# Kernel tuning notes

Hardware: AMD Instinct MI355X
Metric: run time of the kernel (lower is better)

Reference implementation:

```python
import jax, jax.numpy as jnp
import numpy as np

B = 4096
HASH_BITS = 128
TEACHER_DIM = 768
TEMPERATURE = 0.2
CONTRASTIVE_W = 1.0
DISTILL_W = 0.5
QUANT_W = 0.01


def _l2_normalize(x, eps=1e-12):
    # matches torch F.normalize(dim=-1)
    n = jnp.sqrt(jnp.sum(x * x, axis=-1, keepdims=True))
    return x / jnp.maximum(n, eps)


def setup_inputs() -> dict:
    key = jax.random.key(0)
    k1, k2, k3, k4 = jax.random.split(key, 4)
    logits = jax.random.normal(k1, (B, HASH_BITS), dtype=jnp.float32)
    # binary {-1,+1} codes as in the module contract
    hash_codes = jnp.sign(jax.random.normal(k2, (B, HASH_BITS), dtype=jnp.float32))
    hash_codes = jnp.where(hash_codes == 0, 1.0, hash_codes)
    teacher_embed = jax.random.normal(k3, (B, TEACHER_DIM), dtype=jnp.float32)
    # sparse random positives plus self-positives (guarantees each row nonempty)
    rand_pos = jax.random.uniform(k4, (B, B)) < 0.002
    eye = jnp.eye(B, dtype=bool)
    positive_mask = rand_pos | eye
    return {
        "logits": logits,
        "hash_codes": hash_codes,
        "teacher_embed": teacher_embed,
        "positive_mask": positive_mask,
    }


def reference(logits, hash_codes, teacher_embed, positive_mask):
    teacher = _l2_normalize(teacher_embed)

    # ---- contrastive (vectorized form of the per-row python loop) ----
    ln = _l2_normalize(logits)
    sim = (ln @ ln.T) / TEMPERATURE  # [B, B]
    eye = jnp.eye(sim.shape[0], dtype=bool)
    sim_masked = jnp.where(eye, -jnp.inf, sim)
    # per-row stable logsumexp over self-masked similarities
    log_denom = jax.nn.logsumexp(sim_masked, axis=1)  # [B]
    pm = positive_mask.astype(sim.dtype)
    cnt = pm.sum(axis=1)  # [B]
    pos_mean = (sim * pm).sum(axis=1) / jnp.maximum(cnt, 1.0)
    has_pos = cnt > 0
    per_row = jnp.where(has_pos, -pos_mean + log_denom, 0.0)
    num_pos = jnp.maximum(has_pos.sum(), 1)
    loss_cont = per_row.sum() / num_pos.astype(sim.dtype)

    # ---- distillation: hash similarity vs teacher similarity MSE ----
    hash_sim = (hash_codes @ hash_codes.T) / hash_codes.shape[-1]
    teacher_sim = teacher @ teacher.T
    loss_distill = jnp.mean((hash_sim - teacher_sim) ** 2)

    # ---- quantization: push |logits| toward 1 ----
    loss_quant = jnp.mean(jnp.abs(jnp.abs(logits) - 1.0))

    total = (
        CONTRASTIVE_W * loss_cont
        + DISTILL_W * loss_distill
        + QUANT_W * loss_quant
    )
    return total
```

## Files before the change

### kernel.cpp

```cpp
#include <hip/hip_runtime.h>


typedef __bf16 bf16x8 __attribute__((ext_vector_type(8)));
typedef float f32x4 __attribute__((ext_vector_type(4)));

__device__ __forceinline__ unsigned short f2bf(float f) {
  union { float f; unsigned int u; } v; v.f = f;
  unsigned int u = v.u;
  return (unsigned short)((u + 0x7FFFu + ((u >> 16) & 1u)) >> 16);
}

__device__ __forceinline__ void atomAddF(float* p, float v) {
  unsafeAtomicAdd(p, v);
}

__global__ __launch_bounds__(256) void prep(const float* __restrict__ logits,
                                            const float* __restrict__ hash,
                                            const float* __restrict__ teacher,
                                            unsigned short* __restrict__ P,
                                            unsigned char* __restrict__ QT,
                                            float* __restrict__ qpart,
                                            float* __restrict__ rowexp,
                                            float* __restrict__ possum,
                                            float* __restrict__ cntw,
                                            float* __restrict__ accs,
                                            float* __restrict__ Cbuf) {
  __shared__ float rnt[8];
  __shared__ unsigned char QL[8 * 897];
  const int t = threadIdx.x, wave = t >> 6, lane = t & 63;
  const int r0 = (int)blockIdx.x * 8;

  for (int i = t; i < 224; i += 256)
    *(f32x4*)&Cbuf[((size_t)blockIdx.x * 224 + i) * 4] = (f32x4){0.f, 0.f, 0.f, 0.f};
  if (blockIdx.x == 0) {
    if (t < 4) accs[t] = 0.f;
    if (t == 4) *(int*)&accs[4] = 0;
  }

#pragma unroll
  for (int rr = 0; rr < 2; ++rr) {
    const int rl = wave * 2 + rr, r = r0 + rl;
    float ss = 0.f;
#pragma unroll
    for (int i = 0; i < 3; ++i) {
      const float4 v = *(const float4*)&teacher[(size_t)r * 768 + i * 256 + lane * 4];
      ss += v.x * v.x + v.y * v.y + v.z * v.z + v.w * v.w;
    }
    const float2 lv = *(const float2*)&logits[(size_t)r * 128 + lane * 2];
    float ssl = lv.x * lv.x + lv.y * lv.y;
    float qv = fabsf(fabsf(lv.x) - 1.f) + fabsf(fabsf(lv.y) - 1.f);
#pragma unroll
    for (int off = 1; off < 64; off <<= 1) {
      ss += __shfl_xor(ss, off, 64);
      ssl += __shfl_xor(ssl, off, 64);
      qv += __shfl_xor(qv, off, 64);
    }
    const float rnl = 1.f / fmaxf(sqrtf(ssl), 1e-12f);
    const unsigned int pk = (unsigned int)f2bf(lv.x * rnl) |
                            ((unsigned int)f2bf(lv.y * rnl) << 16);
    *(unsigned int*)&P[(size_t)r * 128 + lane * 2] = pk;
    if (lane == 0) {
      rnt[rl] = 11.313708498984761f / fmaxf(sqrtf(ss), 1e-12f);
      qpart[r] = qv;
    }
  }
  if (t < 8) { rowexp[r0 + t] = 0.f; possum[r0 + t] = 0.f; cntw[r0 + t] = 0.f; }
  __syncthreads();

#pragma unroll
  for (int it = 0; it < 2; ++it) {
    const int task = it * 256 + t;
    if (task < 448) {
      const int r = task / 56, cb = task % 56;
      const int r_g = r0 + r;
      unsigned char* dst = &QL[r * 897 + cb * 16];
      if (cb < 8) {
        const float4 v0 = *(const float4*)&hash[(size_t)r_g * 128 + cb * 16];
        const float4 v1 = *(const float4*)&hash[(size_t)r_g * 128 + cb * 16 + 4];
        const float4 v2 = *(const float4*)&hash[(size_t)r_g * 128 + cb * 16 + 8];
        const float4 v3 = *(const float4*)&hash[(size_t)r_g * 128 + cb * 16 + 12];
        const float vv[16] = {v0.x, v0.y, v0.z, v0.w, v1.x, v1.y, v1.z, v1.w,
                              v2.x, v2.y, v2.z, v2.w, v3.x, v3.y, v3.z, v3.w};
#pragma unroll
        for (int k = 0; k < 16; ++k) dst[k] = vv[k] >= 0.f ? 0x38 : 0xB8;
      } else {
        const float sc = rnt[r];
        const int c0 = cb * 16 - 128;
        const float4 v0 = *(const float4*)&teacher[(size_t)r_g * 768 + c0];
        const float4 v1 = *(const float4*)&teacher[(size_t)r_g * 768 + c0 + 4];
        const float4 v2 = *(const float4*)&teacher[(size_t)r_g * 768 + c0 + 8];
        const float4 v3 = *(const float4*)&teacher[(size_t)r_g * 768 + c0 + 12];
        const float vv[16] = {v0.x, v0.y, v0.z, v0.w, v1.x, v1.y, v1.z, v1.w,
                              v2.x, v2.y, v2.z, v2.w, v3.x, v3.y, v3.z, v3.w};
#pragma unroll
        for (int k = 0; k < 16; ++k) {
          const int p8 = __builtin_amdgcn_cvt_pk_fp8_f32(vv[k] * sc, vv[k] * sc,
                                                         0, false);
          dst[k] = (unsigned char)(p8 & 0xFF);
        }
      }
    }
  }
  __syncthreads();

#pragma unroll
  for (int i = 0; i < 4; ++i) {
    const int c = t + 256 * i;
    if (c < 896) {
      unsigned char buf[8];
#pragma unroll
      for (int j = 0; j < 8; ++j) buf[j] = QL[j * 897 + c];
      *(uint2*)&QT[(size_t)c * 4096 + r0] = *(uint2*)buf;
    }
  }
}

#define STAGE_GEN(GA, GB, PITCH, BASE)                                         \
  {                                                                            \
    _Pragma("unroll") for (int it = 0; it < 4; ++it) {                         \
      const int task = it * 256 + t;                                           \
      const int row = task >> 3;                                               \
      const int c16 = (task & 7) ^ (row & 7);                                  \
      const unsigned char* gpA = (GA) + (size_t)row * (PITCH) + c16 * 16;      \
      __builtin_amdgcn_global_load_lds(                                        \
          (const __attribute__((address_space(1))) void*)gpA,                  \
          (__attribute__((address_space(3))) void*)                            \
              &SB[(BASE) + it * 4096 + wave * 1024],                           \
          16, 0, 0);                                                           \
      if (offdiag) {                                                           \
        const unsigned char* gpB = (GB) + (size_t)row * (PITCH) + c16 * 16;    \
        __builtin_amdgcn_global_load_lds(                                      \
            (const __attribute__((address_space(1))) void*)gpB,                \
            (__attribute__((address_space(3))) void*)                         \
                &SB[(BASE) + 16384 + it * 4096 + wave * 1024],                 \
            16, 0, 0);                                                         \
      }                                                                        \
    }                                                                          \
  }

#define MFMA_B(BASE)                                                           \
  {                                                                            \
    _Pragma("unroll") for (int ks = 0; ks < 2; ++ks) {                         \
      const int ph = ((ks * 4 + qd) ^ (l15 & 7)) * 16;                         \
      bf16x8 af[4], bfr[4];                                                    \
      _Pragma("unroll") for (int rt = 0; rt < 4; ++rt)                         \
          af[rt] = *(const bf16x8*)&SB[(BASE) +                                \
                                       (wy * 64 + rt * 16 + l15) * 128 + ph];  \
      _Pragma("unroll") for (int ct = 0; ct < 4; ++ct)                         \
          bfr[ct] = *(const bf16x8*)&SB[(BASE) + boffB +                       \
                                        (wx * 64 + ct * 16 + l15) * 128 + ph]; \
      _Pragma("unroll") for (int rt = 0; rt < 4; ++rt)                         \
          _Pragma("unroll") for (int ct = 0; ct < 4; ++ct) acc[rt][ct] =       \
          __builtin_amdgcn_mfma_f32_16x16x32_bf16(af[rt], bfr[ct],             \
                                                  acc[rt][ct], 0, 0, 0);       \
    }                                                                          \
  }

#define MFMA_Q(BASE)                                                           \
  {                                                                            \
    _Pragma("unroll") for (int ks = 0; ks < 4; ++ks) {                         \
      const int g0 = ks * 4 + qd;                                              \
      const int ph = ((g0 >> 1) ^ (l15 & 7)) * 16 + (g0 & 1) * 8;              \
      long af[4], bfr[4];                                                      \
      _Pragma("unroll") for (int rt = 0; rt < 4; ++rt)                         \
          af[rt] = *(const long*)&SB[(BASE) +                                  \
                                     (wy * 64 + rt * 16 + l15) * 128 + ph];    \
      _Pragma("unroll") for (int ct = 0; ct < 4; ++ct)                         \
          bfr[ct] = *(const long*)&SB[(BASE) + boffB +                         \
                                      (wx * 64 + ct * 16 + l15) * 128 + ph];   \
      _Pragma("unroll") for (int rt = 0; rt < 4; ++rt)                         \
          _Pragma("unroll") for (int ct = 0; ct < 4; ++ct) acc[rt][ct] =       \
          __builtin_amdgcn_mfma_f32_16x16x32_fp8_fp8(af[rt], bfr[ct],          \
                                                     acc[rt][ct], 0, 0, 0);    \
    }                                                                          \
  }

__global__ __launch_bounds__(256, 2) void mega(const unsigned short* __restrict__ P,
                                               const unsigned char* __restrict__ QT,
                                               const void* __restrict__ mask,
                                               float* __restrict__ rowexp,
                                               float* __restrict__ possum,
                                               float* __restrict__ cntw,
                                               float* __restrict__ Cbuf) {
  __shared__ __align__(16) unsigned char SB[65536];
  __shared__ float redrow[128][2];

  const int t = threadIdx.x;
  const int wave = t >> 6, lane = t & 63;
  const int qd = lane >> 4, l15 = lane & 15;
  const int wy = wave >> 1, wx = wave & 1;
  const int b = (int)blockIdx.x;

  f32x4 acc[4][4];
#pragma unroll
  for (int rt = 0; rt < 4; ++rt)
#pragma unroll
    for (int ct = 0; ct < 4; ++ct) acc[rt][ct] = {0.f, 0.f, 0.f, 0.f};

  if (b < 112) {
    const int tile = b >> 2, ksl = b & 3;
    int I = 0, rem = tile;
    while (rem >= 7 - I) { rem -= 7 - I; ++I; }
    const int J = I + rem;
    const bool offdiag = (I != J);
    const int boffB = offdiag ? 16384 : 0;
    const unsigned char* QA = QT + (size_t)I * 128 * 4096 + ksl * 1024;
    const unsigned char* QB = QT + (size_t)J * 128 * 4096 + ksl * 1024;

    STAGE_GEN(QA, QB, 4096, 0);
    __syncthreads();
    for (int kc = 0; kc < 8; ++kc) {
      const int cb = (kc & 1) * 32768;
      if (kc < 7) STAGE_GEN(QA + (kc + 1) * 128, QB + (kc + 1) * 128, 4096,
                            cb ^ 32768);
      MFMA_Q(cb);
      __syncthreads();
    }
    float* Ct = Cbuf + (size_t)tile * 16384;
#pragma unroll
    for (int rt = 0; rt < 4; ++rt)
#pragma unroll
      for (int ct = 0; ct < 4; ++ct)
#pragma unroll
        for (int i = 0; i < 4; ++i)
          atomAddF(&Ct[(rt * 4 + ct) * 1024 + i * 256 + t], acc[rt][ct][i]);
  } else {
    const int bb = b - 112;
    const int l = (bb & 7) * 128 + (bb >> 3);
    const int bi = l >> 5, bj = l & 31;
    const int ti = bi * 128, tj = bj * 128;
    const bool offdiag = (bi != bj);
    const int boffB = offdiag ? 16384 : 0;
    const bool is_byte = ((const unsigned char*)mask)[4097] != 0;

    const unsigned char* Pa = (const unsigned char*)(P + (size_t)ti * 128);
    const unsigned char* Pb = (const unsigned char*)(P + (size_t)tj * 128);

    STAGE_GEN(Pa, Pb, 256, 0);
    __syncthreads();
    STAGE_GEN(Pa + 128, Pb + 128, 256, 32768);
    MFMA_B(0);
    __syncthreads();
    if (is_byte) {
      const unsigned char* m8d = (const unsigned char*)mask + (size_t)ti * 4096 + tj;
#pragma unroll
      for (int it = 0; it < 4; ++it) {
        const int task = it * 256 + t;
        const int row = task >> 3, seg = task & 7;
        __builtin_amdgcn_global_load_lds(
            (const __attribute__((address_space(1))) void*)
                (m8d + (size_t)row * 4096 + seg * 16),
            (__attribute__((address_space(3))) void*)&SB[it * 4096 + wave * 1024],
            16, 0, 0);
      }
    }
    MFMA_B(32768);
    __syncthreads();
    if (!is_byte) {
      const unsigned int* m32 = (const unsigned int*)mask;
#pragma unroll
      for (int it = 0; it < 16; ++it) {
        const int task = it * 256 + t;
        const int row = task >> 5, seg = task & 31;
        const uint4 v = *(const uint4*)&m32[(size_t)(ti + row) * 4096 + tj + seg * 4];
        uchar4 pk;
        pk.x = v.x ? 1 : 0; pk.y = v.y ? 1 : 0;
        pk.z = v.z ? 1 : 0; pk.w = v.w ? 1 : 0;
        *(uchar4*)&SB[row * 128 + seg * 4] = pk;
      }
      __syncthreads();
    }

#pragma unroll
    for (int rt = 0; rt < 4; ++rt) {
#pragma unroll
      for (int r = 0; r < 4; ++r) {
        const int mrow = wy * 64 + rt * 16 + qd * 4 + r;
        const int m = ti + mrow;
        float se = 0.f;
#pragma unroll
        for (int ct = 0; ct < 4; ++ct) {
          const int ncol = wx * 64 + ct * 16 + l15;
          const int n = tj + ncol;
          const float sim = acc[rt][ct][r] * 5.0f;
          const float e = __expf(sim);
          if (m != n) se += e;
          if (SB[mrow * 128 + ncol]) {
            atomAddF(&possum[m], sim);
            atomAddF(&cntw[m], 1.0f);
          }
        }
#pragma unroll
        for (int off = 1; off < 16; off <<= 1) se += __shfl_xor(se, off, 64);
        if (l15 == 0) redrow[mrow][wx] = se;
      }
    }
    __syncthreads();
    if (t < 128) atomAddF(&rowexp[ti + t], redrow[t][0] + redrow[t][1]);
  }
}

__global__ __launch_bounds__(256) void reduce(const float* __restrict__ rowexp,
                                              const float* __restrict__ possum,
                                              const float* __restrict__ cnt,
                                              const float* __restrict__ qpart,
                                              const float* __restrict__ Cbuf,
                                              float* __restrict__ accs,
                                              float* __restrict__ out) {
  const int t = threadIdx.x;
  const int wave = t >> 6, lane = t & 63;
  const int g = (int)blockIdx.x * 256 + t;

  float c = 0.f, q = 0.f, d = 0.f;
  if (g < 4096) {
    c = logf(rowexp[g]) - possum[g] / fmaxf(cnt[g], 1.0f);
    q = qpart[g];
  }
#pragma unroll
  for (int k = 0; k < 7; ++k) {
    const int e4 = g + k * 16384;
    const int tile = e4 >> 12;
    int I = 0, rem = tile;
    while (rem >= 7 - I) { rem -= 7 - I; ++I; }
    const int J = I + rem;
    const float w = (I == J ? 1.f : 2.f) * (((I == 0) == (J == 0)) ? 1.f : -1.f);
    const f32x4 v = *(const f32x4*)&Cbuf[(size_t)e4 * 4];
    d += w * (v[0] * v[0] + v[1] * v[1] + v[2] * v[2] + v[3] * v[3]);
  }
#pragma unroll
  for (int off = 1; off < 64; off <<= 1) {
    c += __shfl_xor(c, off, 64);
    q += __shfl_xor(q, off, 64);
    d += __shfl_xor(d, off, 64);
  }
  __shared__ float sc[4], sq[4], sd[4];
  if (lane == 0) { sc[wave] = c; sq[wave] = q; sd[wave] = d; }
  __syncthreads();
  if (t == 0) {
    atomAddF(&accs[0], sc[0] + sc[1] + sc[2] + sc[3]);
    atomAddF(&accs[1], sq[0] + sq[1] + sq[2] + sq[3]);
    atomAddF(&accs[2], sd[0] + sd[1] + sd[2] + sd[3]);
    __threadfence();
    const int old = atomicAdd((int*)&accs[4], 1);
    if (old == 63) {
      __threadfence();
      const float C = unsafeAtomicAdd(&accs[0], 0.f);
      const float Q = unsafeAtomicAdd(&accs[1], 0.f);
      const float D = unsafeAtomicAdd(&accs[2], 0.f);
      out[0] = C * (1.0f / 4096.0f) + 0.5f * (D * 3.6379788e-12f) +
               0.01f * (Q * (1.0f / 524288.0f));
    }
  }
}

extern "C" void kernel_launch(void* const* d_in, const int* in_sizes, int n_in,
                              void* d_out, int out_size, void* d_ws, size_t ws_size,
                              hipStream_t stream) {
  const float* logits = (const float*)d_in[0];
  const float* hash = (const float*)d_in[1];
  const float* teacher = (const float*)d_in[2];
  const void* mask = d_in[3];
  float* out = (float*)d_out;

  char* ws = (char*)d_ws;
  float* rowexp = (float*)(ws + 0);
  float* possum = (float*)(ws + 16384);
  float* cntw = (float*)(ws + 32768);
  float* qpart = (float*)(ws + 49152);
  float* accs = (float*)(ws + 65536);
  unsigned short* P = (unsigned short*)(ws + 98304);
  unsigned char* QT = (unsigned char*)(ws + 98304 + 1048576);
  float* Cbuf = (float*)(ws + 98304 + 1048576 + 3670016);

  prep<<<512, 256, 0, stream>>>(logits, hash, teacher, P, QT, qpart, rowexp,
                                possum, cntw, accs, Cbuf);
  mega<<<1136, 256, 0, stream>>>(P, QT, mask, rowexp, possum, cntw, Cbuf);
  reduce<<<64, 256, 0, stream>>>(rowexp, possum, cntw, qpart, Cbuf, accs, out);
}
```

Measured before the change: 151.9 us.

## Fuse final reduction into mega kernel via last-block atomic counters

```diff
diff --git a/kernel.cpp b/kernel.cpp
--- a/kernel.cpp
+++ b/kernel.cpp
@@ -12,6 +12,9 @@
 
 __device__ __forceinline__ void atomAddF(float* p, float v) {
   unsafeAtomicAdd(p, v);
+}
+__device__ __forceinline__ float atomReadF(float* p) {
+  return unsafeAtomicAdd(p, 0.f);
 }
 
 __global__ __launch_bounds__(256) void prep(const float* __restrict__ logits,
@@ -24,6 +27,8 @@
                                             float* __restrict__ possum,
                                             float* __restrict__ cntw,
                                             float* __restrict__ accs,
+                                            int* __restrict__ gcnt,
+                                            int* __restrict__ tileCnt,
                                             float* __restrict__ Cbuf) {
   __shared__ float rnt[8];
   __shared__ unsigned char QL[8 * 897];
@@ -33,8 +38,9 @@
   for (int i = t; i < 224; i += 256)
     *(f32x4*)&Cbuf[((size_t)blockIdx.x * 224 + i) * 4] = (f32x4){0.f, 0.f, 0.f, 0.f};
   if (blockIdx.x == 0) {
-    if (t < 4) accs[t] = 0.f;
-    if (t == 4) *(int*)&accs[4] = 0;
+    if (t < 28) tileCnt[t] = 0;
+    if (t == 28) *gcnt = 0;
+    if (t == 29) accs[0] = 0.f;
   }
 
 #pragma unroll
@@ -181,9 +187,16 @@
                                                float* __restrict__ rowexp,
                                                float* __restrict__ possum,
                                                float* __restrict__ cntw,
-                                               float* __restrict__ Cbuf) {
+                                               const float* __restrict__ qpart,
+                                               float* __restrict__ accs,
+                                               int* __restrict__ gcnt,
+                                               int* __restrict__ tileCnt,
+                                               float* __restrict__ Cbuf,
+                                               float* __restrict__ out) {
   __shared__ __align__(16) unsigned char SB[65536];
   __shared__ float redrow[128][2];
+  __shared__ float red4s[4];
+  __shared__ int flagS;
 
   const int t = threadIdx.x;
   const int wave = t >> 6, lane = t & 63;
@@ -224,6 +237,27 @@
 #pragma unroll
         for (int i = 0; i < 4; ++i)
           atomAddF(&Ct[(rt * 4 + ct) * 1024 + i * 256 + t], acc[rt][ct][i]);
+
+    __threadfence();
+    if (t == 0) flagS = atomicAdd(&tileCnt[tile], 1);
+    __syncthreads();
+    if (flagS == 3) {
+      __threadfence();
+      const float w = (I == J ? 1.f : 2.f) *
+                      (((I == 0) == (J == 0)) ? 1.f : -1.f);
+      float d = 0.f;
+      for (int i = t; i < 16384; i += 256) {
+        const float v = atomReadF(&Ct[i]);
+        d += v * v;
+      }
+      d *= w;
+#pragma unroll
+      for (int off = 1; off < 64; off <<= 1) d += __shfl_xor(d, off, 64);
+      if (lane == 0) red4s[wave] = d;
+      __syncthreads();
+      if (t == 0) atomAddF(&accs[0], red4s[0] + red4s[1] + red4s[2] + red4s[3]);
+    }
+    __syncthreads();
   } else {
     const int bb = b - 112;
     const int l = (bb & 7) * 128 + (bb >> 3);
@@ -298,55 +332,31 @@
     __syncthreads();
     if (t < 128) atomAddF(&rowexp[ti + t], redrow[t][0] + redrow[t][1]);
   }
-}
-
-__global__ __launch_bounds__(256) void reduce(const float* __restrict__ rowexp,
-                                              const float* __restrict__ possum,
-                                              const float* __restrict__ cnt,
-                                              const float* __restrict__ qpart,
-                                              const float* __restrict__ Cbuf,
-                                              float* __restrict__ accs,
-                                              float* __restrict__ out) {
-  const int t = threadIdx.x;
-  const int wave = t >> 6, lane = t & 63;
-  const int g = (int)blockIdx.x * 256 + t;
-
-  float c = 0.f, q = 0.f, d = 0.f;
-  if (g < 4096) {
-    c = logf(rowexp[g]) - possum[g] / fmaxf(cnt[g], 1.0f);
-    q = qpart[g];
-  }
-#pragma unroll
-  for (int k = 0; k < 7; ++k) {
-    const int e4 = g + k * 16384;
-    const int tile = e4 >> 12;
-    int I = 0, rem = tile;
-    while (rem >= 7 - I) { rem -= 7 - I; ++I; }
-    const int J = I + rem;
-    const float w = (I == J ? 1.f : 2.f) * (((I == 0) == (J == 0)) ? 1.f : -1.f);
-    const f32x4 v = *(const f32x4*)&Cbuf[(size_t)e4 * 4];
-    d += w * (v[0] * v[0] + v[1] * v[1] + v[2] * v[2] + v[3] * v[3]);
-  }
-#pragma unroll
-  for (int off = 1; off < 64; off <<= 1) {
-    c += __shfl_xor(c, off, 64);
-    q += __shfl_xor(q, off, 64);
-    d += __shfl_xor(d, off, 64);
-  }
-  __shared__ float sc[4], sq[4], sd[4];
-  if (lane == 0) { sc[wave] = c; sq[wave] = q; sd[wave] = d; }
+
+  __threadfence();
+  if (t == 0) flagS = atomicAdd(gcnt, 1);
   __syncthreads();
-  if (t == 0) {
-    atomAddF(&accs[0], sc[0] + sc[1] + sc[2] + sc[3]);
-    atomAddF(&accs[1], sq[0] + sq[1] + sq[2] + sq[3]);
-    atomAddF(&accs[2], sd[0] + sd[1] + sd[2] + sd[3]);
+  if (flagS == 1135) {
     __threadfence();
-    const int old = atomicAdd((int*)&accs[4], 1);
-    if (old == 63) {
-      __threadfence();
-      const float C = unsafeAtomicAdd(&accs[0], 0.f);
-      const float Q = unsafeAtomicAdd(&accs[1], 0.f);
-      const float D = unsafeAtomicAdd(&accs[2], 0.f);
+    float c = 0.f, q = 0.f;
+    for (int m = t; m < 4096; m += 256) {
+      const float re = atomReadF(&rowexp[m]);
+      const float ps = atomReadF(&possum[m]);
+      const float cn = atomReadF(&cntw[m]);
+      c += logf(re) - ps / fmaxf(cn, 1.0f);
+      q += qpart[m];
+    }
+#pragma unroll
+    for (int off = 1; off < 64; off <<= 1) {
+      c += __shfl_xor(c, off, 64);
+      q += __shfl_xor(q, off, 64);
+    }
+    if (lane == 0) { red4s[wave] = c; redrow[wave][0] = q; }
+    __syncthreads();
+    if (t == 0) {
+      const float C = red4s[0] + red4s[1] + red4s[2] + red4s[3];
+      const float Q = redrow[0][0] + redrow[1][0] + redrow[2][0] + redrow[3][0];
+      const float D = atomReadF(&accs[0]);
       out[0] = C * (1.0f / 4096.0f) + 0.5f * (D * 3.6379788e-12f) +
                0.01f * (Q * (1.0f / 524288.0f));
     }
@@ -368,12 +378,14 @@
   float* cntw = (float*)(ws + 32768);
   float* qpart = (float*)(ws + 49152);
   float* accs = (float*)(ws + 65536);
+  int* gcnt = (int*)(ws + 65600);
+  int* tileCnt = (int*)(ws + 65664);
   unsigned short* P = (unsigned short*)(ws + 98304);
   unsigned char* QT = (unsigned char*)(ws + 98304 + 1048576);
   float* Cbuf = (float*)(ws + 98304 + 1048576 + 3670016);
 
   prep<<<512, 256, 0, stream>>>(logits, hash, teacher, P, QT, qpart, rowexp,
-                                possum, cntw, accs, Cbuf);
-  mega<<<1136, 256, 0, stream>>>(P, QT, mask, rowexp, possum, cntw, Cbuf);
-  reduce<<<64, 256, 0, stream>>>(rowexp, possum, cntw, qpart, Cbuf, accs, out);
-}
+                                possum, cntw, accs, gcnt, tileCnt, Cbuf);
+  mega<<<1136, 256, 0, stream>>>(P, QT, mask, rowexp, possum, cntw, qpart,
+                                 accs, gcnt, tileCnt, Cbuf, out);
+}
```

Result: slower. 233.2 us (+53.6%).

## Exploit symmetry of contrastive similarity to compute only upper-triangle tiles

Applied to the files above, without the earlier changes.

```diff
diff --git a/kernel.cpp b/kernel.cpp
--- a/kernel.cpp
+++ b/kernel.cpp
@@ -12,6 +12,9 @@
 
 __device__ __forceinline__ void atomAddF(float* p, float v) {
   unsafeAtomicAdd(p, v);
+}
+__device__ __forceinline__ float atomReadF(float* p) {
+  return unsafeAtomicAdd(p, 0.f);
 }
 
 __global__ __launch_bounds__(256) void prep(const float* __restrict__ logits,
@@ -184,6 +187,7 @@
                                                float* __restrict__ Cbuf) {
   __shared__ __align__(16) unsigned char SB[65536];
   __shared__ float redrow[128][2];
+  __shared__ float redcol[128][2];
 
   const int t = threadIdx.x;
   const int wave = t >> 6, lane = t & 63;
@@ -226,8 +230,10 @@
           atomAddF(&Ct[(rt * 4 + ct) * 1024 + i * 256 + t], acc[rt][ct][i]);
   } else {
     const int bb = b - 112;
-    const int l = (bb & 7) * 128 + (bb >> 3);
-    const int bi = l >> 5, bj = l & 31;
+    const int l = (bb & 7) * 66 + (bb >> 3);
+    int I = 0, rem = l;
+    while (rem >= 32 - I) { rem -= 32 - I; ++I; }
+    const int bi = I, bj = I + rem;
     const int ti = bi * 128, tj = bj * 128;
     const bool offdiag = (bi != bj);
     const int boffB = offdiag ? 16384 : 0;
@@ -242,7 +248,9 @@
     MFMA_B(0);
     __syncthreads();
     if (is_byte) {
-      const unsigned char* m8d = (const unsigned char*)mask + (size_t)ti * 4096 + tj;
+      const unsigned char* m8 = (const unsigned char*)mask;
+      const unsigned char* m8d = m8 + (size_t)ti * 4096 + tj;
+      const unsigned char* m8t = m8 + (size_t)tj * 4096 + ti;
 #pragma unroll
       for (int it = 0; it < 4; ++it) {
         const int task = it * 256 + t;
@@ -252,6 +260,13 @@
                 (m8d + (size_t)row * 4096 + seg * 16),
             (__attribute__((address_space(3))) void*)&SB[it * 4096 + wave * 1024],
             16, 0, 0);
+        if (offdiag)
+          __builtin_amdgcn_global_load_lds(
+              (const __attribute__((address_space(1))) void*)
+                  (m8t + (size_t)row * 4096 + seg * 16),
+              (__attribute__((address_space(3))) void*)
+                  &SB[16384 + it * 4096 + wave * 1024],
+              16, 0, 0);
       }
     }
     MFMA_B(32768);
@@ -267,10 +282,18 @@
         pk.x = v.x ? 1 : 0; pk.y = v.y ? 1 : 0;
         pk.z = v.z ? 1 : 0; pk.w = v.w ? 1 : 0;
         *(uchar4*)&SB[row * 128 + seg * 4] = pk;
+        if (offdiag) {
+          const uint4 w = *(const uint4*)&m32[(size_t)(tj + row) * 4096 + ti + seg * 4];
+          uchar4 pw;
+          pw.x = w.x ? 1 : 0; pw.y = w.y ? 1 : 0;
+          pw.z = w.z ? 1 : 0; pw.w = w.w ? 1 : 0;
+          *(uchar4*)&SB[16384 + row * 128 + seg * 4] = pw;
+        }
       }
       __syncthreads();
     }
 
+    float ce[4] = {0.f, 0.f, 0.f, 0.f};
 #pragma unroll
     for (int rt = 0; rt < 4; ++rt) {
 #pragma unroll
@@ -285,18 +308,35 @@
           const float sim = acc[rt][ct][r] * 5.0f;
           const float e = __expf(sim);
           if (m != n) se += e;
+          if (offdiag) ce[ct] += e;
           if (SB[mrow * 128 + ncol]) {
             atomAddF(&possum[m], sim);
             atomAddF(&cntw[m], 1.0f);
           }
+          if (offdiag && SB[16384 + ncol * 128 + mrow]) {
+            atomAddF(&possum[n], sim);
+            atomAddF(&cntw[n], 1.0f);
+          }
         }
 #pragma unroll
         for (int off = 1; off < 16; off <<= 1) se += __shfl_xor(se, off, 64);
         if (l15 == 0) redrow[mrow][wx] = se;
       }
     }
+    if (offdiag) {
+#pragma unroll
+      for (int ct = 0; ct < 4; ++ct) {
+        float c = ce[ct];
+        c += __shfl_xor(c, 16, 64);
+        c += __shfl_xor(c, 32, 64);
+        if (qd == 0) redcol[wx * 64 + ct * 16 + l15][wy] = c;
+      }
+    }
     __syncthreads();
-    if (t < 128) atomAddF(&rowexp[ti + t], redrow[t][0] + redrow[t][1]);
+    if (t < 128) {
+      atomAddF(&rowexp[ti + t], redrow[t][0] + redrow[t][1]);
+      if (offdiag) atomAddF(&rowexp[tj + t], redcol[t][0] + redcol[t][1]);
+    }
   }
 }
 
@@ -344,9 +384,9 @@
     const int old = atomicAdd((int*)&accs[4], 1);
     if (old == 63) {
       __threadfence();
-      const float C = unsafeAtomicAdd(&accs[0], 0.f);
-      const float Q = unsafeAtomicAdd(&accs[1], 0.f);
-      const float D = unsafeAtomicAdd(&accs[2], 0.f);
+      const float C = atomReadF(&accs[0]);
+      const float Q = atomReadF(&accs[1]);
+      const float D = atomReadF(&accs[2]);
       out[0] = C * (1.0f / 4096.0f) + 0.5f * (D * 3.6379788e-12f) +
                0.01f * (Q * (1.0f / 524288.0f));
     }
@@ -374,6 +414,6 @@
 
   prep<<<512, 256, 0, stream>>>(logits, hash, teacher, P, QT, qpart, rowexp,
                                 possum, cntw, accs, Cbuf);
-  mega<<<1136, 256, 0, stream>>>(P, QT, mask, rowexp, possum, cntw, Cbuf);
+  mega<<<640, 256, 0, stream>>>(P, QT, mask, rowexp, possum, cntw, Cbuf);
   reduce<<<64, 256, 0, stream>>>(rowexp, possum, cntw, qpart, Cbuf, accs, out);
 }
```

New measurement: 176.2 us. 16.0% more time.
